# Optimization experiments

Hardware: AMD Instinct MI355X
Metric: run time of the kernel (lower is better)

Reference implementation:

```python
import jax, jax.numpy as jnp
import numpy as np

N_NODES = 100000


def _gcn_layer(x, src, dst, W, b, n_nodes):
    # x: [N, Cin]; src/dst already include self-loops
    h = x @ W  # [N, Cout]
    deg = jax.ops.segment_sum(jnp.ones_like(dst, dtype=h.dtype), dst,
                              num_segments=n_nodes)  # in-degree incl. self-loop
    dinv = jnp.where(deg > 0, deg ** -0.5, 0.0)
    norm = dinv[src] * dinv[dst]  # [E]
    msg = h[src] * norm[:, None]  # [E, Cout]
    out = jax.ops.segment_sum(msg, dst, num_segments=n_nodes)
    return out + b


def setup_inputs() -> dict:
    key = jax.random.key(0)
    k1, k2, k3, k4, k5, k6, k7 = jax.random.split(key, 7)
    E = 6400000
    x = jax.random.normal(k1, (N_NODES, 5), dtype=jnp.float32)
    edge_index = jax.random.randint(k2, (2, E), 0, N_NODES, dtype=jnp.int64)
    edge_f = jax.random.normal(k3, (E,), dtype=jnp.float32)
    edge_attr = jax.random.normal(k4, (E, 1), dtype=jnp.float32)
    # GCNConv params (glorot-ish scale)
    W1 = jax.random.normal(k5, (5, 8), dtype=jnp.float32) * (1.0 / np.sqrt(5))
    b1 = jnp.zeros((8,), dtype=jnp.float32)
    W2 = jax.random.normal(k6, (8, 5), dtype=jnp.float32) * (1.0 / np.sqrt(8))
    b2 = jnp.zeros((5,), dtype=jnp.float32)
    return {"x": x, "edge_index": edge_index, "edge_f": edge_f,
            "edge_attr": edge_attr, "W1": W1, "b1": b1, "W2": W2, "b2": b2}


def reference(x, edge_index, edge_f, edge_attr, W1, b1, W2, b2):
    n = x.shape[0]
    loops = jnp.arange(n, dtype=edge_index.dtype)
    src = jnp.concatenate([edge_index[0], loops])  # add self-loops (PyG default)
    dst = jnp.concatenate([edge_index[1], loops])
    h = _gcn_layer(x, src, dst, W1, b1, n)
    h = _gcn_layer(h, src, dst, W2, b2, n)
    return h
```

## Files before the change

### kernel.cpp

```cpp
#include <hip/hip_runtime.h>


#define TPB 256
#define VPB 256
#define B_BITS 8
#define MAXB 512
#define CAP 17408
#define NBLK_E 256
#define EPB 25000
#define SCT 1024
#define DGT 1024

typedef int int4e __attribute__((ext_vector_type(4)));
__device__ __forceinline__ int4e ntload4(const int* p) {
    return __builtin_nontemporal_load((const int4e*)p);
}
__device__ __forceinline__ int ntload(const int* p) {
    return __builtin_nontemporal_load(p);
}

__global__ void k_init(int B, int* __restrict__ bpos) {
    int b = blockIdx.x * blockDim.x + threadIdx.x;
    if (b < B) bpos[b] = b * CAP;
}

__global__ __launch_bounds__(SCT) void k_scat(const int* __restrict__ src,
        const int* __restrict__ dst, int E, int B,
        int* __restrict__ bpos, int* __restrict__ pairs) {
    __shared__ int sorted[EPB];
    __shared__ int hist[MAXB], scn[MAXB], cur[MAXB], gbase[MAXB];
    int t = threadIdx.x;
    for (int i = t; i < MAXB; i += SCT) hist[i] = 0;
    __syncthreads();
    int lo = blockIdx.x * EPB;
    int n = min(E - lo, EPB);
    int n4 = n & ~3;
    for (int i = t * 4; i < n4; i += SCT * 4) {
        int4e d4 = ntload4(dst + lo + i);
        atomicAdd(&hist[d4.x >> B_BITS], 1);
        atomicAdd(&hist[d4.y >> B_BITS], 1);
        atomicAdd(&hist[d4.z >> B_BITS], 1);
        atomicAdd(&hist[d4.w >> B_BITS], 1);
    }
    for (int i = n4 + t; i < n; i += SCT)
        atomicAdd(&hist[dst[lo + i] >> B_BITS], 1);
    __syncthreads();
    if (t < MAXB) scn[t] = hist[t];
    __syncthreads();
    for (int off = 1; off < MAXB; off <<= 1) {
        int v = (t >= off && t < MAXB) ? scn[t - off] : 0;
        __syncthreads();
        if (t < MAXB) scn[t] += v;
        __syncthreads();
    }
    if (t < MAXB) {
        int h = hist[t];
        cur[t] = scn[t] - h;
        gbase[t] = (t < B && h) ? atomicAdd(&bpos[t], h) : 0;
    }
    __syncthreads();
    for (int i = t * 4; i < n4; i += SCT * 4) {
        int4e d4 = ntload4(dst + lo + i);
        int4e s4 = ntload4(src + lo + i);
        int p;
        p = atomicAdd(&cur[d4.x >> B_BITS], 1); sorted[p] = (s4.x << B_BITS) | (d4.x & (VPB - 1));
        p = atomicAdd(&cur[d4.y >> B_BITS], 1); sorted[p] = (s4.y << B_BITS) | (d4.y & (VPB - 1));
        p = atomicAdd(&cur[d4.z >> B_BITS], 1); sorted[p] = (s4.z << B_BITS) | (d4.z & (VPB - 1));
        p = atomicAdd(&cur[d4.w >> B_BITS], 1); sorted[p] = (s4.w << B_BITS) | (d4.w & (VPB - 1));
    }
    for (int i = n4 + t; i < n; i += SCT) {
        int d = dst[lo + i], s = src[lo + i];
        int p = atomicAdd(&cur[d >> B_BITS], 1);
        sorted[p] = (s << B_BITS) | (d & (VPB - 1));
    }
    __syncthreads();
    int wave = t >> 6, lane = t & 63;
    for (int b2 = wave; b2 < B; b2 += (SCT >> 6)) {
        int h = hist[b2];
        int st = scn[b2] - h;
        int gb = gbase[b2];
        for (int j = lane; j < h; j += 64)
            pairs[gb + j] = sorted[st + j];
    }
}

__global__ __launch_bounds__(DGT) void k_degh1(const int* __restrict__ pairs,
        const int* __restrict__ bpos, int N,
        const float* __restrict__ x, const float* __restrict__ W1,
        unsigned int* __restrict__ jinfo, float* __restrict__ dinv,
        float* __restrict__ h1s) {
    __shared__ int hist[VPB];
    __shared__ int scn[VPB];
    int t = threadIdx.x, b = blockIdx.x;
    if (t < VPB) hist[t] = 0;
    __syncthreads();
    int base = b * CAP;
    int n = bpos[b] - base, n4 = n & ~3;
    for (int i = t * 4; i < n4; i += DGT * 4) {
        int4e p = ntload4(pairs + base + i);
        atomicAdd(&hist[p.x & (VPB - 1)], 1);
        atomicAdd(&hist[p.y & (VPB - 1)], 1);
        atomicAdd(&hist[p.z & (VPB - 1)], 1);
        atomicAdd(&hist[p.w & (VPB - 1)], 1);
    }
    for (int i = n4 + t; i < n; i += DGT)
        atomicAdd(&hist[pairs[base + i] & (VPB - 1)], 1);
    __syncthreads();
    if (t < VPB) scn[t] = hist[t];
    __syncthreads();
    for (int off = 1; off < VPB; off <<= 1) {
        int v = (t >= off && t < VPB) ? scn[t - off] : 0;
        __syncthreads();
        if (t < VPB) scn[t] += v;
        __syncthreads();
    }
    int node = b * VPB + t;
    if (t < VPB && node < N) {
        int h = hist[t];
        int start = base + scn[t] - h;
        jinfo[node] = ((unsigned int)start << 9) | (unsigned int)h;
        float di = rsqrtf((float)(h + 1));
        dinv[node] = di;
        float xi[5];
#pragma unroll
        for (int c = 0; c < 5; ++c) xi[c] = x[(size_t)node * 5 + c];
        float o[8];
#pragma unroll
        for (int j = 0; j < 8; ++j) {
            float hh = 0.f;
#pragma unroll
            for (int c = 0; c < 5; ++c) hh += xi[c] * W1[c * 8 + j];
            o[j] = hh * di;
        }
        float4* hp = (float4*)(h1s + (size_t)node * 8);
        hp[0] = make_float4(o[0], o[1], o[2], o[3]);
        hp[1] = make_float4(o[4], o[5], o[6], o[7]);
    }
}

__global__ __launch_bounds__(1024) void k_agg1(const int* __restrict__ pairs_,
        const int* __restrict__ bpos, const unsigned int* __restrict__ jinfo,
        const float* __restrict__ h1s, const float* __restrict__ dinv,
        const float* __restrict__ b1, const float* __restrict__ W2,
        float* __restrict__ h2s, int N) {
    __shared__ int csr[CAP];
    __shared__ int js[VPB], ct[VPB], cur[VPB];
    int* pairs = (int*)pairs_;
    int t = threadIdx.x, b = blockIdx.x;
    int base = b * CAP;
    if (t < VPB) {
        int node = b * VPB + t;
        int s = 0, c = 0;
        if (node < N) {
            unsigned int u = jinfo[node];
            s = (int)(u >> 9) - base;
            c = (int)(u & 511u);
        }
        js[t] = s; ct[t] = c; cur[t] = s;
    }
    __syncthreads();
    int n = bpos[b] - base, n4 = n & ~3;
    for (int i = t * 4; i < n4; i += 1024 * 4) {
        int4e p = ntload4(pairs + base + i);
        int q;
        q = atomicAdd(&cur[p.x & (VPB - 1)], 1); csr[q] = p.x >> B_BITS;
        q = atomicAdd(&cur[p.y & (VPB - 1)], 1); csr[q] = p.y >> B_BITS;
        q = atomicAdd(&cur[p.z & (VPB - 1)], 1); csr[q] = p.z >> B_BITS;
        q = atomicAdd(&cur[p.w & (VPB - 1)], 1); csr[q] = p.w >> B_BITS;
    }
    for (int i = n4 + t; i < n; i += 1024) {
        int p = pairs[base + i];
        int q = atomicAdd(&cur[p & (VPB - 1)], 1);
        csr[q] = p >> B_BITS;
    }
    __syncthreads();
    for (int i = t; i < n; i += 1024)
        __builtin_nontemporal_store(csr[i], pairs + base + i);
    int lane = t & 3, ln = t >> 2;
    int node = b * VPB + ln;
    if (node >= N) return;
    int s0 = js[ln], cn = ct[ln];
    float a0 = 0.f, a1 = 0.f, a2 = 0.f, a3 = 0.f,
          a4 = 0.f, a5 = 0.f, a6 = 0.f, a7 = 0.f;
    int j = lane;
    for (; j + 4 < cn; j += 8) {
        int sA = csr[s0 + j];
        int sB = csr[s0 + j + 4];
        const float4* pA = (const float4*)(h1s + (size_t)sA * 8);
        const float4* pB = (const float4*)(h1s + (size_t)sB * 8);
        float4 xA = pA[0], yA = pA[1];
        float4 xB = pB[0], yB = pB[1];
        a0 += xA.x + xB.x; a1 += xA.y + xB.y; a2 += xA.z + xB.z; a3 += xA.w + xB.w;
        a4 += yA.x + yB.x; a5 += yA.y + yB.y; a6 += yA.z + yB.z; a7 += yA.w + yB.w;
    }
    if (j < cn) {
        int sA = csr[s0 + j];
        const float4* pA = (const float4*)(h1s + (size_t)sA * 8);
        float4 xA = pA[0], yA = pA[1];
        a0 += xA.x; a1 += xA.y; a2 += xA.z; a3 += xA.w;
        a4 += yA.x; a5 += yA.y; a6 += yA.z; a7 += yA.w;
    }
#pragma unroll
    for (int d = 1; d < 4; d <<= 1) {
        a0 += __shfl_xor(a0, d); a1 += __shfl_xor(a1, d);
        a2 += __shfl_xor(a2, d); a3 += __shfl_xor(a3, d);
        a4 += __shfl_xor(a4, d); a5 += __shfl_xor(a5, d);
        a6 += __shfl_xor(a6, d); a7 += __shfl_xor(a7, d);
    }
    const float4* sp = (const float4*)(h1s + (size_t)node * 8);
    float4 sx = sp[0], sy = sp[1];
    float di = dinv[node];
    float o[8];
    o[0] = (a0 + sx.x) * di + b1[0]; o[1] = (a1 + sx.y) * di + b1[1];
    o[2] = (a2 + sx.z) * di + b1[2]; o[3] = (a3 + sx.w) * di + b1[3];
    o[4] = (a4 + sy.x) * di + b1[4]; o[5] = (a5 + sy.y) * di + b1[5];
    o[6] = (a6 + sy.z) * di + b1[6]; o[7] = (a7 + sy.w) * di + b1[7];
    {
        float h = 0.f;
#pragma unroll
        for (int jj = 0; jj < 8; ++jj) h += o[jj] * W2[jj * 5 + lane];
        h2s[(size_t)node * 8 + lane] = h * di;
        if (lane == 0) {
            float h4 = 0.f;
#pragma unroll
            for (int jj = 0; jj < 8; ++jj) h4 += o[jj] * W2[jj * 5 + 4];
            h2s[(size_t)node * 8 + 4] = h4 * di;
        }
    }
}

__global__ __launch_bounds__(TPB) void k_agg2(const int* __restrict__ pairs,
        const unsigned int* __restrict__ jinfo, const float* __restrict__ h2s,
        const float* __restrict__ dinv, const float* __restrict__ b2,
        float* __restrict__ out, int N) {
    int gid = blockIdx.x * blockDim.x + threadIdx.x;
    int node = gid >> 3, lane = gid & 7;
    if (node >= N) return;
    unsigned int u = jinfo[node];
    int jsa = (int)(u >> 9), cn = (int)(u & 511u);
    float a0 = 0.f, a1 = 0.f, a2 = 0.f, a3 = 0.f, a4 = 0.f;
    int j = lane;
    for (; j + 8 < cn; j += 16) {
        int sA = ntload(pairs + jsa + j);
        int sB = ntload(pairs + jsa + j + 8);
        const float4* pA = (const float4*)(h2s + (size_t)sA * 8);
        const float4* pB = (const float4*)(h2s + (size_t)sB * 8);
        float4 xA = pA[0]; float eA = h2s[(size_t)sA * 8 + 4];
        float4 xB = pB[0]; float eB = h2s[(size_t)sB * 8 + 4];
        a0 += xA.x + xB.x; a1 += xA.y + xB.y; a2 += xA.z + xB.z;
        a3 += xA.w + xB.w; a4 += eA + eB;
    }
    if (j < cn) {
        int sA = ntload(pairs + jsa + j);
        const float4* pA = (const float4*)(h2s + (size_t)sA * 8);
        float4 xA = pA[0]; float eA = h2s[(size_t)sA * 8 + 4];
        a0 += xA.x; a1 += xA.y; a2 += xA.z; a3 += xA.w; a4 += eA;
    }
#pragma unroll
    for (int d = 1; d < 8; d <<= 1) {
        a0 += __shfl_xor(a0, d); a1 += __shfl_xor(a1, d);
        a2 += __shfl_xor(a2, d); a3 += __shfl_xor(a3, d);
        a4 += __shfl_xor(a4, d);
    }
    if (lane == 0) {
        float di = dinv[node];
        const float* sr = h2s + (size_t)node * 8;
        float* op = out + (size_t)node * 5;
        op[0] = (a0 + sr[0]) * di + b2[0];
        op[1] = (a1 + sr[1]) * di + b2[1];
        op[2] = (a2 + sr[2]) * di + b2[2];
        op[3] = (a3 + sr[3]) * di + b2[3];
        op[4] = (a4 + sr[4]) * di + b2[4];
    }
}

extern "C" void kernel_launch(void* const* d_in, const int* in_sizes, int n_in,
                              void* d_out, int out_size, void* d_ws, size_t ws_size,
                              hipStream_t stream) {
    const float* x   = (const float*)d_in[0];
    const int*  eidx = (const int*)d_in[1];
    const float* W1 = (const float*)d_in[4];
    const float* b1 = (const float*)d_in[5];
    const float* W2 = (const float*)d_in[6];
    const float* b2 = (const float*)d_in[7];
    float* out = (float*)d_out;

    const int N = in_sizes[0] / 5;
    const int E = in_sizes[1] / 2;
    const int* src = eidx;
    const int* dst = eidx + E;

    const int B = (N + VPB - 1) / VPB;

    int*   pairs = (int*)d_ws;
    float* h1s   = (float*)(pairs + (size_t)B * CAP);
    float* h2s   = h1s + (size_t)8 * N;
    float* dinv  = h2s + (size_t)8 * N;
    unsigned int* jinfo = (unsigned int*)(dinv + N);
    int*   bpos  = (int*)(jinfo + N);

    const int g8N = (8 * N + TPB - 1) / TPB;

    k_init <<<(B + TPB - 1) / TPB, TPB, 0, stream>>>(B, bpos);
    k_scat <<<NBLK_E, SCT, 0, stream>>>(src, dst, E, B, bpos, pairs);
    k_degh1<<<B, DGT, 0, stream>>>(pairs, bpos, N, x, W1, jinfo, dinv, h1s);
    k_agg1 <<<B, 1024, 0, stream>>>(pairs, bpos, jinfo, h1s, dinv, b1, W2, h2s, N);
    k_agg2 <<<g8N, TPB, 0, stream>>>(pairs, jinfo, h2s, dinv, b2, out, N);
}
```

Baseline: 254.4 us.

## Fuse degree, layer-1 and layer-2 aggregation into one cooperative kernel

Replaces the three post-scatter kernels with a single cooperative kernel. Each block builds its CSR bucket in shared memory once, then uses grid-wide syncs between the degree/h1 stage, the layer-1 aggregation and the layer-2 aggregation. This removes two kernel launch boundaries and the repeated global re-reads of the pairs/jinfo arrays, and it switches to 4-lane-per-node gathers. The cost is that the cooperative launch needs all B (~391) blocks of 512 threads with about 70KB of shared memory each to be resident at once. If that launch fails, the code falls back to the old three-kernel path.

```diff
diff --git a/kernel.cpp b/kernel.cpp
--- a/kernel.cpp
+++ b/kernel.cpp
@@ -1,4 +1,7 @@
 #include <hip/hip_runtime.h>
+#include <hip/hip_cooperative_groups.h>
+
+namespace cg = cooperative_groups;
 
 
 #define TPB 256
@@ -81,6 +84,179 @@
         int gb = gbase[b2];
         for (int j = lane; j < h; j += 64)
             pairs[gb + j] = sorted[st + j];
+    }
+}
+
+__global__ __launch_bounds__(512, 4) void k_fused(const int* __restrict__ pairs,
+        const int* __restrict__ bpos, int N,
+        const float* __restrict__ x, const float* __restrict__ W1,
+        const float* __restrict__ b1, const float* __restrict__ W2,
+        const float* __restrict__ b2,
+        float* __restrict__ h1s, float* __restrict__ h2s,
+        float* __restrict__ out) {
+    cg::grid_group grid = cg::this_grid();
+    __shared__ int csr[CAP];
+    __shared__ int hist[VPB], scn[VPB], cur[VPB], js[VPB], ct[VPB];
+    __shared__ float sdinv[VPB];
+    int t = threadIdx.x, b = blockIdx.x;
+    int base = b * CAP;
+    int n = bpos[b] - base, n4 = n & ~3;
+
+    if (t < VPB) hist[t] = 0;
+    __syncthreads();
+    for (int i = t * 4; i < n4; i += 512 * 4) {
+        int4e p = ntload4(pairs + base + i);
+        atomicAdd(&hist[p.x & (VPB - 1)], 1);
+        atomicAdd(&hist[p.y & (VPB - 1)], 1);
+        atomicAdd(&hist[p.z & (VPB - 1)], 1);
+        atomicAdd(&hist[p.w & (VPB - 1)], 1);
+    }
+    for (int i = n4 + t; i < n; i += 512)
+        atomicAdd(&hist[pairs[base + i] & (VPB - 1)], 1);
+    __syncthreads();
+    if (t < VPB) scn[t] = hist[t];
+    __syncthreads();
+    for (int off = 1; off < VPB; off <<= 1) {
+        int v = (t >= off && t < VPB) ? scn[t - off] : 0;
+        __syncthreads();
+        if (t < VPB) scn[t] += v;
+        __syncthreads();
+    }
+    if (t < VPB) {
+        int h = hist[t];
+        int st = scn[t] - h;
+        cur[t] = st; js[t] = st; ct[t] = h;
+        int node = b * VPB + t;
+        if (node < N) {
+            float di = rsqrtf((float)(h + 1));
+            sdinv[t] = di;
+            float xi[5];
+#pragma unroll
+            for (int c = 0; c < 5; ++c) xi[c] = x[(size_t)node * 5 + c];
+            float o[8];
+#pragma unroll
+            for (int j = 0; j < 8; ++j) {
+                float hh = 0.f;
+#pragma unroll
+                for (int c = 0; c < 5; ++c) hh += xi[c] * W1[c * 8 + j];
+                o[j] = hh * di;
+            }
+            float4* hp = (float4*)(h1s + (size_t)node * 8);
+            hp[0] = make_float4(o[0], o[1], o[2], o[3]);
+            hp[1] = make_float4(o[4], o[5], o[6], o[7]);
+        }
+    }
+    __syncthreads();
+    for (int i = t * 4; i < n4; i += 512 * 4) {
+        int4e p = ntload4(pairs + base + i);
+        int q;
+        q = atomicAdd(&cur[p.x & (VPB - 1)], 1); csr[q] = p.x >> B_BITS;
+        q = atomicAdd(&cur[p.y & (VPB - 1)], 1); csr[q] = p.y >> B_BITS;
+        q = atomicAdd(&cur[p.z & (VPB - 1)], 1); csr[q] = p.z >> B_BITS;
+        q = atomicAdd(&cur[p.w & (VPB - 1)], 1); csr[q] = p.w >> B_BITS;
+    }
+    for (int i = n4 + t; i < n; i += 512) {
+        int p = pairs[base + i];
+        int q = atomicAdd(&cur[p & (VPB - 1)], 1);
+        csr[q] = p >> B_BITS;
+    }
+    grid.sync();
+
+    int lane = t & 3;
+#pragma unroll 1
+    for (int pass = 0; pass < 2; ++pass) {
+        int ln = (t >> 2) + pass * 128;
+        int node = b * VPB + ln;
+        if (node >= N) continue;
+        int s0 = js[ln], cn = ct[ln];
+        float a0 = 0.f, a1 = 0.f, a2 = 0.f, a3 = 0.f,
+              a4 = 0.f, a5 = 0.f, a6 = 0.f, a7 = 0.f;
+        int j = lane;
+        for (; j + 4 < cn; j += 8) {
+            int sA = csr[s0 + j];
+            int sB = csr[s0 + j + 4];
+            const float4* pA = (const float4*)(h1s + (size_t)sA * 8);
+            const float4* pB = (const float4*)(h1s + (size_t)sB * 8);
+            float4 xA = pA[0], yA = pA[1];
+            float4 xB = pB[0], yB = pB[1];
+            a0 += xA.x + xB.x; a1 += xA.y + xB.y; a2 += xA.z + xB.z; a3 += xA.w + xB.w;
+            a4 += yA.x + yB.x; a5 += yA.y + yB.y; a6 += yA.z + yB.z; a7 += yA.w + yB.w;
+        }
+        if (j < cn) {
+            int sA = csr[s0 + j];
+            const float4* pA = (const float4*)(h1s + (size_t)sA * 8);
+            float4 xA = pA[0], yA = pA[1];
+            a0 += xA.x; a1 += xA.y; a2 += xA.z; a3 += xA.w;
+            a4 += yA.x; a5 += yA.y; a6 += yA.z; a7 += yA.w;
+        }
+#pragma unroll
+        for (int d = 1; d < 4; d <<= 1) {
+            a0 += __shfl_xor(a0, d); a1 += __shfl_xor(a1, d);
+            a2 += __shfl_xor(a2, d); a3 += __shfl_xor(a3, d);
+            a4 += __shfl_xor(a4, d); a5 += __shfl_xor(a5, d);
+            a6 += __shfl_xor(a6, d); a7 += __shfl_xor(a7, d);
+        }
+        const float4* sp = (const float4*)(h1s + (size_t)node * 8);
+        float4 sx = sp[0], sy = sp[1];
+        float di = sdinv[ln];
+        float o[8];
+        o[0] = (a0 + sx.x) * di + b1[0]; o[1] = (a1 + sx.y) * di + b1[1];
+        o[2] = (a2 + sx.z) * di + b1[2]; o[3] = (a3 + sx.w) * di + b1[3];
+        o[4] = (a4 + sy.x) * di + b1[4]; o[5] = (a5 + sy.y) * di + b1[5];
+        o[6] = (a6 + sy.z) * di + b1[6]; o[7] = (a7 + sy.w) * di + b1[7];
+        float h = 0.f;
+#pragma unroll
+        for (int jj = 0; jj < 8; ++jj) h += o[jj] * W2[jj * 5 + lane];
+        h2s[(size_t)node * 8 + lane] = h * di;
+        if (lane == 0) {
+            float h4 = 0.f;
+#pragma unroll
+            for (int jj = 0; jj < 8; ++jj) h4 += o[jj] * W2[jj * 5 + 4];
+            h2s[(size_t)node * 8 + 4] = h4 * di;
+        }
+    }
+    grid.sync();
+
+#pragma unroll 1
+    for (int pass = 0; pass < 2; ++pass) {
+        int ln = (t >> 2) + pass * 128;
+        int node = b * VPB + ln;
+        if (node >= N) continue;
+        int s0 = js[ln], cn = ct[ln];
+        float a0 = 0.f, a1 = 0.f, a2 = 0.f, a3 = 0.f, a4 = 0.f;
+        int j = lane;
+        for (; j + 4 < cn; j += 8) {
+            int sA = csr[s0 + j];
+            int sB = csr[s0 + j + 4];
+            const float4* pA = (const float4*)(h2s + (size_t)sA * 8);
+            const float4* pB = (const float4*)(h2s + (size_t)sB * 8);
+            float4 xA = pA[0]; float eA = h2s[(size_t)sA * 8 + 4];
+            float4 xB = pB[0]; float eB = h2s[(size_t)sB * 8 + 4];
+            a0 += xA.x + xB.x; a1 += xA.y + xB.y; a2 += xA.z + xB.z;
+            a3 += xA.w + xB.w; a4 += eA + eB;
+        }
+        if (j < cn) {
+            int sA = csr[s0 + j];
+            const float4* pA = (const float4*)(h2s + (size_t)sA * 8);
+            float4 xA = pA[0]; float eA = h2s[(size_t)sA * 8 + 4];
+            a0 += xA.x; a1 += xA.y; a2 += xA.z; a3 += xA.w; a4 += eA;
+        }
+#pragma unroll
+        for (int d = 1; d < 4; d <<= 1) {
+            a0 += __shfl_xor(a0, d); a1 += __shfl_xor(a1, d);
+            a2 += __shfl_xor(a2, d); a3 += __shfl_xor(a3, d);
+            a4 += __shfl_xor(a4, d);
+        }
+        if (lane == 0) {
+            float di = sdinv[ln];
+            const float* sr = h2s + (size_t)node * 8;
+            float* op = out + (size_t)node * 5;
+            op[0] = (a0 + sr[0]) * di + b2[0];
+            op[1] = (a1 + sr[1]) * di + b2[1];
+            op[2] = (a2 + sr[2]) * di + b2[2];
+            op[3] = (a3 + sr[3]) * di + b2[3];
+            op[4] = (a4 + sr[4]) * di + b2[4];
+        }
     }
 }
 
@@ -285,8 +461,8 @@
     const float* b2 = (const float*)d_in[7];
     float* out = (float*)d_out;
 
-    const int N = in_sizes[0] / 5;
-    const int E = in_sizes[1] / 2;
+    int N = in_sizes[0] / 5;
+    int E = in_sizes[1] / 2;
     const int* src = eidx;
     const int* dst = eidx + E;
 
@@ -299,11 +475,18 @@
     unsigned int* jinfo = (unsigned int*)(dinv + N);
     int*   bpos  = (int*)(jinfo + N);
 
-    const int g8N = (8 * N + TPB - 1) / TPB;
-
-    k_init <<<(B + TPB - 1) / TPB, TPB, 0, stream>>>(B, bpos);
-    k_scat <<<NBLK_E, SCT, 0, stream>>>(src, dst, E, B, bpos, pairs);
-    k_degh1<<<B, DGT, 0, stream>>>(pairs, bpos, N, x, W1, jinfo, dinv, h1s);
-    k_agg1 <<<B, 1024, 0, stream>>>(pairs, bpos, jinfo, h1s, dinv, b1, W2, h2s, N);
-    k_agg2 <<<g8N, TPB, 0, stream>>>(pairs, jinfo, h2s, dinv, b2, out, N);
-}
+    k_init<<<(B + TPB - 1) / TPB, TPB, 0, stream>>>(B, bpos);
+    k_scat<<<NBLK_E, SCT, 0, stream>>>(src, dst, E, B, bpos, pairs);
+
+    void* args[] = {(void*)&pairs, (void*)&bpos, (void*)&N,
+                    (void*)&x, (void*)&W1, (void*)&b1, (void*)&W2, (void*)&b2,
+                    (void*)&h1s, (void*)&h2s, (void*)&out};
+    hipError_t err = hipLaunchCooperativeKernel((void*)k_fused, dim3(B),
+                                                dim3(512), args, 0, stream);
+    if (err != hipSuccess) {
+        const int g8N = (8 * N + TPB - 1) / TPB;
+        k_degh1<<<B, DGT, 0, stream>>>(pairs, bpos, N, x, W1, jinfo, dinv, h1s);
+        k_agg1 <<<B, 1024, 0, stream>>>(pairs, bpos, jinfo, h1s, dinv, b1, W2, h2s, N);
+        k_agg2 <<<g8N, TPB, 0, stream>>>(pairs, jinfo, h2s, dinv, b2, out, N);
+    }
+}
```

Result: slower. 343.5 us (+35.0%).

## Aggregate 5-wide scaled inputs before W1 and retune scatter block sizes

Applied to the files above, without the earlier changes.

Applies the first layer's linear transform after aggregation instead of before, so the gather in k_agg1 reads 5 scaled input features per neighbour instead of 8 transformed ones. W1 is then applied once per node after the reduction. The separate dinv array is dropped and recomputed with rsqrt from the degree count. The scatter and degree kernels also switch to half the threads per block with twice as many scatter blocks, which changes occupancy and the shared sort size per block.

```diff
diff --git a/kernel.cpp b/kernel.cpp
--- a/kernel.cpp
+++ b/kernel.cpp
@@ -6,10 +6,10 @@
 #define B_BITS 8
 #define MAXB 512
 #define CAP 17408
-#define NBLK_E 256
-#define EPB 25000
-#define SCT 1024
-#define DGT 1024
+#define NBLK_E 512
+#define EPB 12500
+#define SCT 512
+#define DGT 512
 
 typedef int int4e __attribute__((ext_vector_type(4)));
 __device__ __forceinline__ int4e ntload4(const int* p) {
@@ -84,11 +84,10 @@
     }
 }
 
-__global__ __launch_bounds__(DGT) void k_degh1(const int* __restrict__ pairs,
+__global__ __launch_bounds__(DGT) void k_degxs(const int* __restrict__ pairs,
         const int* __restrict__ bpos, int N,
-        const float* __restrict__ x, const float* __restrict__ W1,
-        unsigned int* __restrict__ jinfo, float* __restrict__ dinv,
-        float* __restrict__ h1s) {
+        const float* __restrict__ x,
+        unsigned int* __restrict__ jinfo, float* __restrict__ xs) {
     __shared__ int hist[VPB];
     __shared__ int scn[VPB];
     int t = threadIdx.x, b = blockIdx.x;
@@ -120,28 +119,17 @@
         int start = base + scn[t] - h;
         jinfo[node] = ((unsigned int)start << 9) | (unsigned int)h;
         float di = rsqrtf((float)(h + 1));
-        dinv[node] = di;
-        float xi[5];
-#pragma unroll
-        for (int c = 0; c < 5; ++c) xi[c] = x[(size_t)node * 5 + c];
-        float o[8];
-#pragma unroll
-        for (int j = 0; j < 8; ++j) {
-            float hh = 0.f;
-#pragma unroll
-            for (int c = 0; c < 5; ++c) hh += xi[c] * W1[c * 8 + j];
-            o[j] = hh * di;
-        }
-        float4* hp = (float4*)(h1s + (size_t)node * 8);
-        hp[0] = make_float4(o[0], o[1], o[2], o[3]);
-        hp[1] = make_float4(o[4], o[5], o[6], o[7]);
+        const float* xp = x + (size_t)node * 5;
+        float4 v4 = make_float4(xp[0] * di, xp[1] * di, xp[2] * di, xp[3] * di);
+        *(float4*)(xs + (size_t)node * 8) = v4;
+        xs[(size_t)node * 8 + 4] = xp[4] * di;
     }
 }
 
 __global__ __launch_bounds__(1024) void k_agg1(const int* __restrict__ pairs_,
         const int* __restrict__ bpos, const unsigned int* __restrict__ jinfo,
-        const float* __restrict__ h1s, const float* __restrict__ dinv,
-        const float* __restrict__ b1, const float* __restrict__ W2,
+        const float* __restrict__ xs, const float* __restrict__ b1,
+        const float* __restrict__ W1, const float* __restrict__ W2,
         float* __restrict__ h2s, int N) {
     __shared__ int csr[CAP];
     __shared__ int js[VPB], ct[VPB], cur[VPB];
@@ -180,50 +168,53 @@
     int node = b * VPB + ln;
     if (node >= N) return;
     int s0 = js[ln], cn = ct[ln];
-    float a0 = 0.f, a1 = 0.f, a2 = 0.f, a3 = 0.f,
-          a4 = 0.f, a5 = 0.f, a6 = 0.f, a7 = 0.f;
+    float a0 = 0.f, a1 = 0.f, a2 = 0.f, a3 = 0.f, a4 = 0.f;
     int j = lane;
     for (; j + 4 < cn; j += 8) {
         int sA = csr[s0 + j];
         int sB = csr[s0 + j + 4];
-        const float4* pA = (const float4*)(h1s + (size_t)sA * 8);
-        const float4* pB = (const float4*)(h1s + (size_t)sB * 8);
-        float4 xA = pA[0], yA = pA[1];
-        float4 xB = pB[0], yB = pB[1];
-        a0 += xA.x + xB.x; a1 += xA.y + xB.y; a2 += xA.z + xB.z; a3 += xA.w + xB.w;
-        a4 += yA.x + yB.x; a5 += yA.y + yB.y; a6 += yA.z + yB.z; a7 += yA.w + yB.w;
+        const float* pA = xs + (size_t)sA * 8;
+        const float* pB = xs + (size_t)sB * 8;
+        float4 xA = *(const float4*)pA; float eA = pA[4];
+        float4 xB = *(const float4*)pB; float eB = pB[4];
+        a0 += xA.x + xB.x; a1 += xA.y + xB.y; a2 += xA.z + xB.z;
+        a3 += xA.w + xB.w; a4 += eA + eB;
     }
     if (j < cn) {
         int sA = csr[s0 + j];
-        const float4* pA = (const float4*)(h1s + (size_t)sA * 8);
-        float4 xA = pA[0], yA = pA[1];
-        a0 += xA.x; a1 += xA.y; a2 += xA.z; a3 += xA.w;
-        a4 += yA.x; a5 += yA.y; a6 += yA.z; a7 += yA.w;
+        const float* pA = xs + (size_t)sA * 8;
+        float4 xA = *(const float4*)pA;
+        a0 += xA.x; a1 += xA.y; a2 += xA.z; a3 += xA.w; a4 += pA[4];
     }
 #pragma unroll
     for (int d = 1; d < 4; d <<= 1) {
         a0 += __shfl_xor(a0, d); a1 += __shfl_xor(a1, d);
         a2 += __shfl_xor(a2, d); a3 += __shfl_xor(a3, d);
-        a4 += __shfl_xor(a4, d); a5 += __shfl_xor(a5, d);
-        a6 += __shfl_xor(a6, d); a7 += __shfl_xor(a7, d);
-    }
-    const float4* sp = (const float4*)(h1s + (size_t)node * 8);
-    float4 sx = sp[0], sy = sp[1];
-    float di = dinv[node];
-    float o[8];
-    o[0] = (a0 + sx.x) * di + b1[0]; o[1] = (a1 + sx.y) * di + b1[1];
-    o[2] = (a2 + sx.z) * di + b1[2]; o[3] = (a3 + sx.w) * di + b1[3];
-    o[4] = (a4 + sy.x) * di + b1[4]; o[5] = (a5 + sy.y) * di + b1[5];
-    o[6] = (a6 + sy.z) * di + b1[6]; o[7] = (a7 + sy.w) * di + b1[7];
+        a4 += __shfl_xor(a4, d);
+    }
+    const float* sp = xs + (size_t)node * 8;
+    float4 sx = *(const float4*)sp;
+    float tc[5];
+    tc[0] = a0 + sx.x; tc[1] = a1 + sx.y; tc[2] = a2 + sx.z;
+    tc[3] = a3 + sx.w; tc[4] = a4 + sp[4];
+    float di = rsqrtf((float)(cn + 1));
+    float o1[8];
+#pragma unroll
+    for (int jj = 0; jj < 8; ++jj) {
+        float h = 0.f;
+#pragma unroll
+        for (int c = 0; c < 5; ++c) h += tc[c] * W1[c * 8 + jj];
+        o1[jj] = h * di + b1[jj];
+    }
     {
         float h = 0.f;
 #pragma unroll
-        for (int jj = 0; jj < 8; ++jj) h += o[jj] * W2[jj * 5 + lane];
+        for (int jj = 0; jj < 8; ++jj) h += o1[jj] * W2[jj * 5 + lane];
         h2s[(size_t)node * 8 + lane] = h * di;
         if (lane == 0) {
             float h4 = 0.f;
 #pragma unroll
-            for (int jj = 0; jj < 8; ++jj) h4 += o[jj] * W2[jj * 5 + 4];
+            for (int jj = 0; jj < 8; ++jj) h4 += o1[jj] * W2[jj * 5 + 4];
             h2s[(size_t)node * 8 + 4] = h4 * di;
         }
     }
@@ -231,8 +222,7 @@
 
 __global__ __launch_bounds__(TPB) void k_agg2(const int* __restrict__ pairs,
         const unsigned int* __restrict__ jinfo, const float* __restrict__ h2s,
-        const float* __restrict__ dinv, const float* __restrict__ b2,
-        float* __restrict__ out, int N) {
+        const float* __restrict__ b2, float* __restrict__ out, int N) {
     int gid = blockIdx.x * blockDim.x + threadIdx.x;
     int node = gid >> 3, lane = gid & 7;
     if (node >= N) return;
@@ -243,18 +233,18 @@
     for (; j + 8 < cn; j += 16) {
         int sA = ntload(pairs + jsa + j);
         int sB = ntload(pairs + jsa + j + 8);
-        const float4* pA = (const float4*)(h2s + (size_t)sA * 8);
-        const float4* pB = (const float4*)(h2s + (size_t)sB * 8);
-        float4 xA = pA[0]; float eA = h2s[(size_t)sA * 8 + 4];
-        float4 xB = pB[0]; float eB = h2s[(size_t)sB * 8 + 4];
+        const float* pA = h2s + (size_t)sA * 8;
+        const float* pB = h2s + (size_t)sB * 8;
+        float4 xA = *(const float4*)pA; float eA = pA[4];
+        float4 xB = *(const float4*)pB; float eB = pB[4];
         a0 += xA.x + xB.x; a1 += xA.y + xB.y; a2 += xA.z + xB.z;
         a3 += xA.w + xB.w; a4 += eA + eB;
     }
     if (j < cn) {
         int sA = ntload(pairs + jsa + j);
-        const float4* pA = (const float4*)(h2s + (size_t)sA * 8);
-        float4 xA = pA[0]; float eA = h2s[(size_t)sA * 8 + 4];
-        a0 += xA.x; a1 += xA.y; a2 += xA.z; a3 += xA.w; a4 += eA;
+        const float* pA = h2s + (size_t)sA * 8;
+        float4 xA = *(const float4*)pA;
+        a0 += xA.x; a1 += xA.y; a2 += xA.z; a3 += xA.w; a4 += pA[4];
     }
 #pragma unroll
     for (int d = 1; d < 8; d <<= 1) {
@@ -263,7 +253,7 @@
         a4 += __shfl_xor(a4, d);
     }
     if (lane == 0) {
-        float di = dinv[node];
+        float di = rsqrtf((float)(cn + 1));
         const float* sr = h2s + (size_t)node * 8;
         float* op = out + (size_t)node * 5;
         op[0] = (a0 + sr[0]) * di + b2[0];
@@ -279,8 +269,8 @@
                               hipStream_t stream) {
     const float* x   = (const float*)d_in[0];
     const int*  eidx = (const int*)d_in[1];
+    const float* b1 = (const float*)d_in[5];
     const float* W1 = (const float*)d_in[4];
-    const float* b1 = (const float*)d_in[5];
     const float* W2 = (const float*)d_in[6];
     const float* b2 = (const float*)d_in[7];
     float* out = (float*)d_out;
@@ -293,17 +283,16 @@
     const int B = (N + VPB - 1) / VPB;
 
     int*   pairs = (int*)d_ws;
-    float* h1s   = (float*)(pairs + (size_t)B * CAP);
-    float* h2s   = h1s + (size_t)8 * N;
-    float* dinv  = h2s + (size_t)8 * N;
-    unsigned int* jinfo = (unsigned int*)(dinv + N);
+    float* xs    = (float*)(pairs + (size_t)B * CAP);
+    float* h2s   = xs + (size_t)8 * N;
+    unsigned int* jinfo = (unsigned int*)(h2s + (size_t)8 * N);
     int*   bpos  = (int*)(jinfo + N);
 
     const int g8N = (8 * N + TPB - 1) / TPB;
 
     k_init <<<(B + TPB - 1) / TPB, TPB, 0, stream>>>(B, bpos);
     k_scat <<<NBLK_E, SCT, 0, stream>>>(src, dst, E, B, bpos, pairs);
-    k_degh1<<<B, DGT, 0, stream>>>(pairs, bpos, N, x, W1, jinfo, dinv, h1s);
-    k_agg1 <<<B, 1024, 0, stream>>>(pairs, bpos, jinfo, h1s, dinv, b1, W2, h2s, N);
-    k_agg2 <<<g8N, TPB, 0, stream>>>(pairs, jinfo, h2s, dinv, b2, out, N);
-}
+    k_degxs<<<B, DGT, 0, stream>>>(pairs, bpos, N, x, jinfo, xs);
+    k_agg1 <<<B, 1024, 0, stream>>>(pairs, bpos, jinfo, xs, b1, W1, W2, h2s, N);
+    k_agg2 <<<g8N, TPB, 0, stream>>>(pairs, jinfo, h2s, b2, out, N);
+}
```

Measured after the change: 258.3 us. Within noise of the previous version (+1.5%).
